# Performance work log

Measured on AMD Instinct MI355X. Metric: run time of the kernel, lower is better.

## Reference

```python
import jax, jax.numpy as jnp
import numpy as np

NUM_EXPERTS = 8

def setup_inputs() -> dict:
    key = jax.random.key(0)
    k1, k2, k3, k4, k5 = jax.random.split(key, 5)
    T, D, H, O, E, K = 4096, 1024, 2048, 1024, NUM_EXPERTS, 2
    hidden_states = jax.random.normal(k1, (T, D), dtype=jnp.float32)
    top_k_indices = jax.random.randint(k2, (T, K), 0, E, dtype=jnp.int64)
    top_k_weights = jax.random.uniform(k3, (T, K), dtype=jnp.float32)
    gate_up_proj = jax.random.normal(k4, (E, 2 * H, D), dtype=jnp.float32) * 0.02
    down_proj = jax.random.normal(k5, (E, O, H), dtype=jnp.float32) * 0.02
    return {
        "hidden_states": hidden_states,
        "top_k_indices": top_k_indices,
        "top_k_weights": top_k_weights,
        "gate_up_proj": gate_up_proj,
        "down_proj": down_proj,
    }


def _moe(hidden_states, top_k_weights, gate_up_proj, down_proj, top_k_indices):
    # Mathematically identical to the torch per-token-gather loop, expressed as
    # dense all-expert compute + sparse combine (non-selected experts get weight 0).
    T = hidden_states.shape[0]
    E = gate_up_proj.shape[0]
    # [T, E, 2H]
    gate_up = jnp.einsum('td,ehd->teh', hidden_states, gate_up_proj)
    gate, up = jnp.split(gate_up, 2, axis=-1)
    h = jax.nn.silu(gate) * up  # [T, E, H]
    expert_out = jnp.einsum('teh,eoh->teo', h, down_proj)  # [T, E, O]
    # combine weights: scatter top-k routing weights into [T, E]
    combine = jnp.zeros((T, E), dtype=hidden_states.dtype)
    rows = jnp.arange(T)[:, None]
    combine = combine.at[rows, top_k_indices].add(top_k_weights)
    return jnp.einsum('teo,te->to', expert_out, combine)


def reference(hidden_states, top_k_indices, top_k_weights, gate_up_proj, down_proj):
    return _moe(hidden_states, top_k_weights, gate_up_proj, down_proj, top_k_indices)
```

## Files before the change

### kernel.cpp

```cpp
#include <hip/hip_runtime.h>
#include <stdint.h>

#define TOKS 4096
#define DIM  1024
#define HID  2048
#define OUTD 1024
#define NE   8
#define MP   9216
#define NBR  72

typedef __bf16 bf16;
typedef bf16 bf16x8 __attribute__((ext_vector_type(8)));
typedef float f32x4 __attribute__((ext_vector_type(4)));
typedef __attribute__((address_space(1))) void gvoid;
typedef __attribute__((address_space(3))) void lvoid;

#define WGU_OFF  0ull
#define WD_OFF   (WGU_OFF + 67108864ull)
#define XG_OFF   (WD_OFF  + 33554432ull)
#define H_OFF    (XG_OFF  + 18874368ull)
#define TK_OFF   (H_OFF   + 37748736ull)
#define META_OFF (TK_OFF  + 36864ull)
#define T2S_OFF  (META_OFF + 1024ull)
#define O0_OFF   WGU_OFF
#define O1_OFF   (WGU_OFF + 18874368ull)

__device__ __forceinline__ unsigned short f2bf(float f) {
  union { float f; unsigned u; } v; v.f = f;
  unsigned r = (v.u + 0x7FFFu + ((v.u >> 16) & 1u)) >> 16;
  return (unsigned short)r;
}
__device__ __forceinline__ float bf2f(unsigned short h) {
  union { unsigned u; float f; } v; v.u = ((unsigned)h) << 16; return v.f;
}
__device__ __forceinline__ unsigned pack2(float a, float b) {
  return (unsigned)f2bf(a) | ((unsigned)f2bf(b) << 16);
}
__device__ __forceinline__ void cp16(const void* g, void* l) {
  __builtin_amdgcn_global_load_lds((gvoid*)(void*)g, (lvoid*)l, 16, 0, 0);
}

__global__ __launch_bounds__(1024) void route_kernel(const int* __restrict__ idx,
                                                     int* __restrict__ table,
                                                     int* __restrict__ slot_token,
                                                     int* __restrict__ tok2slot) {
  __shared__ int cnt[NE], offs[NE], cur[NE];
  const int tid = threadIdx.x, lane = tid & 63;
  for (int i = tid; i < MP; i += 1024) slot_token[i] = -1;
  if (tid < NE) cnt[tid] = 0;
  __syncthreads();
  int myE[8];
#pragma unroll
  for (int c = 0; c < 8; ++c) myE[c] = idx[c * 1024 + tid];
#pragma unroll
  for (int c = 0; c < 8; ++c) {
    int e = myE[c];
#pragma unroll
    for (int ex = 0; ex < NE; ++ex) {
      unsigned long long m = __ballot(e == ex);
      if (lane == 0 && m) atomicAdd(&cnt[ex], __popcll(m));
    }
  }
  __syncthreads();
  if (tid == 0) {
    int cum = 0;
    for (int e = 0; e < NE; ++e) {
      offs[e] = cum; cur[e] = 0;
      int nb = (cnt[e] + 127) >> 7;
      int bb = cum >> 7;
      for (int b = 0; b < nb; ++b) table[bb + b] = e;
      cum += nb << 7;
    }
    for (int b = cum >> 7; b < NBR; ++b) table[b] = -1;
  }
  __syncthreads();
#pragma unroll
  for (int c = 0; c < 8; ++c) {
    int e = myE[c];
    int pos = 0;
#pragma unroll
    for (int ex = 0; ex < NE; ++ex) {
      unsigned long long m = __ballot(e == ex);
      if (e == ex) {
        int rank = __popcll(m & ((1ull << lane) - 1ull));
        int leader = __ffsll(m) - 1;
        int base = 0;
        if (lane == leader) base = atomicAdd(&cur[ex], __popcll(m));
        base = __shfl(base, leader);
        pos = offs[ex] + base + rank;
      }
    }
    slot_token[pos] = (c * 1024 + tid) >> 1;
    tok2slot[c * 1024 + tid] = pos;
  }
}

#define GATHER_B 4608
__global__ void prep_kernel(const float* __restrict__ X, const int* __restrict__ slot_token,
                            uint4* __restrict__ Xg,
                            const float4* __restrict__ srcGu, uint2* __restrict__ dstGu,
                            const float4* __restrict__ srcD, uint2* __restrict__ dstD) {
  int bx = blockIdx.x;
  if (bx < GATHER_B) {
    int gid = bx * 256 + threadIdx.x;
    int row = gid >> 7, j = (gid & 127) << 3;
    int t = slot_token[row];
    uint4 o;
    if (t >= 0) {
      const float4* p = (const float4*)(X + (size_t)t * DIM + j);
      float4 a = p[0], b = p[1];
      o.x = pack2(a.x, a.y); o.y = pack2(a.z, a.w);
      o.z = pack2(b.x, b.y); o.w = pack2(b.z, b.w);
    } else {
      o = uint4{0u, 0u, 0u, 0u};
    }
    Xg[gid] = o;
  } else {
    const int n1 = NE * 2 * HID * DIM / 4;
    int i = (bx - GATHER_B) * 256 + threadIdx.x;
    float4 v; uint2* dp;
    if (i < n1) { v = srcGu[i]; dp = dstGu + i; }
    else        { v = srcD[i - n1]; dp = dstD + (i - n1); }
    uint2 o; o.x = pack2(v.x, v.y); o.y = pack2(v.z, v.w);
    *dp = o;
  }
}

__global__ void combine_kernel(const unsigned short* __restrict__ O0,
                               const unsigned short* __restrict__ O1,
                               const int* __restrict__ tok2slot,
                               const float* __restrict__ wts, float4* __restrict__ out) {
  int t = blockIdx.x, c = threadIdx.x;
  int s0 = tok2slot[2 * t], s1 = tok2slot[2 * t + 1];
  float w0 = wts[2 * t], w1 = wts[2 * t + 1];
  uint2 a0 = ((const uint2*)(O0 + (size_t)s0 * OUTD))[c];
  uint2 b0 = ((const uint2*)(O1 + (size_t)s0 * OUTD))[c];
  uint2 a1 = ((const uint2*)(O0 + (size_t)s1 * OUTD))[c];
  uint2 b1 = ((const uint2*)(O1 + (size_t)s1 * OUTD))[c];
  float4 o;
  o.x = w0 * (bf2f(a0.x & 0xFFFF) + bf2f(b0.x & 0xFFFF)) + w1 * (bf2f(a1.x & 0xFFFF) + bf2f(b1.x & 0xFFFF));
  o.y = w0 * (bf2f(a0.x >> 16)    + bf2f(b0.x >> 16))    + w1 * (bf2f(a1.x >> 16)    + bf2f(b1.x >> 16));
  o.z = w0 * (bf2f(a0.y & 0xFFFF) + bf2f(b0.y & 0xFFFF)) + w1 * (bf2f(a1.y & 0xFFFF) + bf2f(b1.y & 0xFFFF));
  o.w = w0 * (bf2f(a0.y >> 16)    + bf2f(b0.y >> 16))    + w1 * (bf2f(a1.y >> 16)    + bf2f(b1.y >> 16));
  out[(size_t)t * (OUTD / 4) + c] = o;
}

__global__ __launch_bounds__(256) void gemm1_kernel(
    const unsigned short* __restrict__ Xg,
    const unsigned short* __restrict__ Wgu,
    unsigned short* __restrict__ Hbuf,
    const int* __restrict__ table) {
  int e = table[blockIdx.y];
  if (e < 0) return;
  const int tid = threadIdx.x;
  const int lane = tid & 63, wave = tid >> 6;
  const int wm = wave >> 1, wn = wave & 1;
  const int lr = lane & 15, quad = lane >> 4;

  __shared__ bf16 As[128 * 64];
  __shared__ bf16 Bg[64 * 64];
  __shared__ bf16 Bu[64 * 64];

  const unsigned short* A_base  = Xg  + (size_t)blockIdx.y * 128 * DIM;
  const unsigned short* Wg_base = Wgu + (size_t)e * 2 * HID * DIM + (size_t)(blockIdx.x * 64) * DIM;
  const unsigned short* Wu_base = Wg_base + (size_t)HID * DIM;

  f32x4 accg[4][2] = {}; f32x4 accu[4][2] = {};

  for (int kt = 0; kt < DIM / 64; ++kt) {
    const int kb = kt * 64;
#pragma unroll
    for (int i = 0; i < 4; ++i) {
      int s = i * 256 + tid, row = s >> 3, pc = s & 7, gc = pc ^ (row & 7);
      cp16(A_base + (size_t)row * DIM + kb + gc * 8, (void*)(As + row * 64 + pc * 8));
    }
#pragma unroll
    for (int i = 0; i < 2; ++i) {
      int s = i * 256 + tid, row = s >> 3, pc = s & 7, gc = pc ^ (row & 7);
      cp16(Wg_base + (size_t)row * DIM + kb + gc * 8, (void*)(Bg + row * 64 + pc * 8));
      cp16(Wu_base + (size_t)row * DIM + kb + gc * 8, (void*)(Bu + row * 64 + pc * 8));
    }
    __syncthreads();
#pragma unroll
    for (int ks = 0; ks < 2; ++ks) {
      bf16x8 a[4], bg[2], bu[2];
#pragma unroll
      for (int i = 0; i < 4; ++i) {
        int row = wm * 64 + i * 16 + lr;
        int pc = (ks * 4 + quad) ^ (row & 7);
        a[i] = *(const bf16x8*)(As + row * 64 + pc * 8);
      }
#pragma unroll
      for (int j = 0; j < 2; ++j) {
        int row = wn * 32 + j * 16 + lr;
        int pc = (ks * 4 + quad) ^ (row & 7);
        bg[j] = *(const bf16x8*)(Bg + row * 64 + pc * 8);
        bu[j] = *(const bf16x8*)(Bu + row * 64 + pc * 8);
      }
#pragma unroll
      for (int i = 0; i < 4; ++i)
#pragma unroll
        for (int j = 0; j < 2; ++j) {
          accg[i][j] = __builtin_amdgcn_mfma_f32_16x16x32_bf16(a[i], bg[j], accg[i][j], 0, 0, 0);
          accu[i][j] = __builtin_amdgcn_mfma_f32_16x16x32_bf16(a[i], bu[j], accu[i][j], 0, 0, 0);
        }
    }
    __syncthreads();
  }

  const int rowBase = blockIdx.y * 128 + wm * 64;
  const int colBase = blockIdx.x * 64 + wn * 32;
#pragma unroll
  for (int i = 0; i < 4; ++i)
#pragma unroll
    for (int r = 0; r < 4; ++r) {
      int row = rowBase + i * 16 + quad * 4 + r;
#pragma unroll
      for (int j = 0; j < 2; ++j) {
        float g = accg[i][j][r], u = accu[i][j][r];
        float s = g / (1.0f + __expf(-g));
        Hbuf[(size_t)row * HID + colBase + j * 16 + lr] = f2bf(s * u);
      }
    }
}

__global__ __launch_bounds__(256) void gemm2_kernel(
    const unsigned short* __restrict__ Hbuf,
    const unsigned short* __restrict__ Wd,
    unsigned short* __restrict__ O0,
    unsigned short* __restrict__ O1,
    const int* __restrict__ table) {
  int e = table[blockIdx.y];
  if (e < 0) return;
  const int tid = threadIdx.x;
  const int lane = tid & 63, wave = tid >> 6;
  const int wm = wave >> 1, wn = wave & 1;
  const int lr = lane & 15, quad = lane >> 4;
  const int kslice = blockIdx.z;

  __shared__ bf16 As[128 * 64];
  __shared__ bf16 Bs[128 * 64];

  const unsigned short* A_base = Hbuf + (size_t)blockIdx.y * 128 * HID + kslice * (HID / 2);
  const unsigned short* B_base = Wd + (size_t)e * OUTD * HID + (size_t)(blockIdx.x * 128) * HID
                               + kslice * (HID / 2);

  f32x4 acc[4][4] = {};

  for (int kt = 0; kt < (HID / 2) / 64; ++kt) {
    const int kb = kt * 64;
#pragma unroll
    for (int i = 0; i < 4; ++i) {
      int s = i * 256 + tid, row = s >> 3, pc = s & 7, gc = pc ^ (row & 7);
      cp16(A_base + (size_t)row * HID + kb + gc * 8, (void*)(As + row * 64 + pc * 8));
      cp16(B_base + (size_t)row * HID + kb + gc * 8, (void*)(Bs + row * 64 + pc * 8));
    }
    __syncthreads();
#pragma unroll
    for (int ks = 0; ks < 2; ++ks) {
      bf16x8 a[4], b[4];
#pragma unroll
      for (int i = 0; i < 4; ++i) {
        int row = wm * 64 + i * 16 + lr;
        int pc = (ks * 4 + quad) ^ (row & 7);
        a[i] = *(const bf16x8*)(As + row * 64 + pc * 8);
      }
#pragma unroll
      for (int j = 0; j < 4; ++j) {
        int row = wn * 64 + j * 16 + lr;
        int pc = (ks * 4 + quad) ^ (row & 7);
        b[j] = *(const bf16x8*)(Bs + row * 64 + pc * 8);
      }
#pragma unroll
      for (int i = 0; i < 4; ++i)
#pragma unroll
        for (int j = 0; j < 4; ++j)
          acc[i][j] = __builtin_amdgcn_mfma_f32_16x16x32_bf16(a[i], b[j], acc[i][j], 0, 0, 0);
    }
    __syncthreads();
  }

  unsigned short* O = kslice ? O1 : O0;
  const int rowBase = blockIdx.y * 128 + wm * 64;
  const int colBase = blockIdx.x * 128 + wn * 64;
#pragma unroll
  for (int i = 0; i < 4; ++i)
#pragma unroll
    for (int r = 0; r < 4; ++r) {
      int row = rowBase + i * 16 + quad * 4 + r;
      unsigned short* Orow = O + (size_t)row * OUTD + colBase;
#pragma unroll
      for (int j = 0; j < 4; ++j)
        Orow[j * 16 + lr] = f2bf(acc[i][j][r]);
    }
}

extern "C" void kernel_launch(void* const* d_in, const int* in_sizes, int n_in,
                              void* d_out, int out_size, void* d_ws, size_t ws_size,
                              hipStream_t stream) {
  const float* X     = (const float*)d_in[0];
  const int*   idx   = (const int*)d_in[1];
  const float* wts   = (const float*)d_in[2];
  const float* WguF  = (const float*)d_in[3];
  const float* WdF   = (const float*)d_in[4];
  float* out = (float*)d_out;

  char* base = (char*)d_ws;
  unsigned short* Wgu = (unsigned short*)(base + WGU_OFF);
  unsigned short* Wd  = (unsigned short*)(base + WD_OFF);
  unsigned short* Xg  = (unsigned short*)(base + XG_OFF);
  unsigned short* Hb  = (unsigned short*)(base + H_OFF);
  unsigned short* O0  = (unsigned short*)(base + O0_OFF);
  unsigned short* O1  = (unsigned short*)(base + O1_OFF);
  int* slot_token = (int*)(base + TK_OFF);
  int* table      = (int*)(base + META_OFF);
  int* tok2slot   = (int*)(base + T2S_OFF);

  route_kernel<<<1, 1024, 0, stream>>>(idx, table, slot_token, tok2slot);
  {
    const int convB = (NE * 2 * HID * DIM + NE * OUTD * HID) / 4 / 256;
    prep_kernel<<<GATHER_B + convB, 256, 0, stream>>>(X, slot_token, (uint4*)Xg,
        (const float4*)WguF, (uint2*)Wgu, (const float4*)WdF, (uint2*)Wd);
  }
  gemm1_kernel<<<dim3(HID / 64, NBR), 256, 0, stream>>>(Xg, Wgu, Hb, table);
  gemm2_kernel<<<dim3(OUTD / 128, NBR, 2), 256, 0, stream>>>(Hb, Wd, O0, O1, table);
  combine_kernel<<<TOKS, 256, 0, stream>>>(O0, O1, tok2slot, wts, (float4*)out);
}
```

Baseline: 434.4 us.

## Double-buffer LDS in expert GEMMs and merge weight conversion into routing launch

Both grouped GEMMs now use two LDS buffers so the global-to-LDS copies for the next K tile are issued before computing the current one, aiming to hide load latency. The fp32-to-bf16 weight conversion is moved into the routing launch so it runs alongside the single-block routing work, and the token gather becomes a separate kernel. Doubled LDS usage may lower occupancy per CU.

Result: slower. 452.2 us (+4.1%).

```diff
diff --git a/kernel.cpp b/kernel.cpp
--- a/kernel.cpp
+++ b/kernel.cpp
@@ -40,10 +40,22 @@
   __builtin_amdgcn_global_load_lds((gvoid*)(void*)g, (lvoid*)l, 16, 0, 0);
 }
 
-__global__ __launch_bounds__(1024) void route_kernel(const int* __restrict__ idx,
-                                                     int* __restrict__ table,
-                                                     int* __restrict__ slot_token,
-                                                     int* __restrict__ tok2slot) {
+#define CONVB ((NE * 2 * HID * DIM + NE * OUTD * HID) / 4 / 1024)
+__global__ __launch_bounds__(1024) void route_conv_kernel(
+    const int* __restrict__ idx, int* __restrict__ table,
+    int* __restrict__ slot_token, int* __restrict__ tok2slot,
+    const float4* __restrict__ srcGu, uint2* __restrict__ dstGu,
+    const float4* __restrict__ srcD, uint2* __restrict__ dstD) {
+  if (blockIdx.x != 0) {
+    const int n1 = NE * 2 * HID * DIM / 4;
+    int i = (int)(blockIdx.x - 1) * 1024 + threadIdx.x;
+    float4 v; uint2* dp;
+    if (i < n1) { v = srcGu[i]; dp = dstGu + i; }
+    else        { v = srcD[i - n1]; dp = dstD + (i - n1); }
+    uint2 o; o.x = pack2(v.x, v.y); o.y = pack2(v.z, v.w);
+    *dp = o;
+    return;
+  }
   __shared__ int cnt[NE], offs[NE], cur[NE];
   const int tid = threadIdx.x, lane = tid & 63;
   for (int i = tid; i < MP; i += 1024) slot_token[i] = -1;
@@ -96,34 +108,22 @@
 }
 
 #define GATHER_B 4608
-__global__ void prep_kernel(const float* __restrict__ X, const int* __restrict__ slot_token,
-                            uint4* __restrict__ Xg,
-                            const float4* __restrict__ srcGu, uint2* __restrict__ dstGu,
-                            const float4* __restrict__ srcD, uint2* __restrict__ dstD) {
-  int bx = blockIdx.x;
-  if (bx < GATHER_B) {
-    int gid = bx * 256 + threadIdx.x;
-    int row = gid >> 7, j = (gid & 127) << 3;
-    int t = slot_token[row];
-    uint4 o;
-    if (t >= 0) {
-      const float4* p = (const float4*)(X + (size_t)t * DIM + j);
-      float4 a = p[0], b = p[1];
-      o.x = pack2(a.x, a.y); o.y = pack2(a.z, a.w);
-      o.z = pack2(b.x, b.y); o.w = pack2(b.z, b.w);
-    } else {
-      o = uint4{0u, 0u, 0u, 0u};
-    }
-    Xg[gid] = o;
+__global__ void gather_kernel(const float* __restrict__ X,
+                              const int* __restrict__ slot_token,
+                              uint4* __restrict__ Xg) {
+  int gid = blockIdx.x * 256 + threadIdx.x;
+  int row = gid >> 7, j = (gid & 127) << 3;
+  int t = slot_token[row];
+  uint4 o;
+  if (t >= 0) {
+    const float4* p = (const float4*)(X + (size_t)t * DIM + j);
+    float4 a = p[0], b = p[1];
+    o.x = pack2(a.x, a.y); o.y = pack2(a.z, a.w);
+    o.z = pack2(b.x, b.y); o.w = pack2(b.z, b.w);
   } else {
-    const int n1 = NE * 2 * HID * DIM / 4;
-    int i = (bx - GATHER_B) * 256 + threadIdx.x;
-    float4 v; uint2* dp;
-    if (i < n1) { v = srcGu[i]; dp = dstGu + i; }
-    else        { v = srcD[i - n1]; dp = dstD + (i - n1); }
-    uint2 o; o.x = pack2(v.x, v.y); o.y = pack2(v.z, v.w);
-    *dp = o;
-  }
+    o = uint4{0u, 0u, 0u, 0u};
+  }
+  Xg[gid] = o;
 }
 
 __global__ void combine_kernel(const unsigned short* __restrict__ O0,
@@ -157,9 +157,9 @@
   const int wm = wave >> 1, wn = wave & 1;
   const int lr = lane & 15, quad = lane >> 4;
 
-  __shared__ bf16 As[128 * 64];
-  __shared__ bf16 Bg[64 * 64];
-  __shared__ bf16 Bu[64 * 64];
+  __shared__ bf16 As[2][128 * 64];
+  __shared__ bf16 Bg[2][64 * 64];
+  __shared__ bf16 Bu[2][64 * 64];
 
   const unsigned short* A_base  = Xg  + (size_t)blockIdx.y * 128 * DIM;
   const unsigned short* Wg_base = Wgu + (size_t)e * 2 * HID * DIM + (size_t)(blockIdx.x * 64) * DIM;
@@ -167,20 +167,22 @@
 
   f32x4 accg[4][2] = {}; f32x4 accu[4][2] = {};
 
-  for (int kt = 0; kt < DIM / 64; ++kt) {
+  auto stage = [&](int buf, int kt) {
     const int kb = kt * 64;
 #pragma unroll
     for (int i = 0; i < 4; ++i) {
       int s = i * 256 + tid, row = s >> 3, pc = s & 7, gc = pc ^ (row & 7);
-      cp16(A_base + (size_t)row * DIM + kb + gc * 8, (void*)(As + row * 64 + pc * 8));
+      cp16(A_base + (size_t)row * DIM + kb + gc * 8, (void*)(&As[buf][row * 64 + pc * 8]));
     }
 #pragma unroll
     for (int i = 0; i < 2; ++i) {
       int s = i * 256 + tid, row = s >> 3, pc = s & 7, gc = pc ^ (row & 7);
-      cp16(Wg_base + (size_t)row * DIM + kb + gc * 8, (void*)(Bg + row * 64 + pc * 8));
-      cp16(Wu_base + (size_t)row * DIM + kb + gc * 8, (void*)(Bu + row * 64 + pc * 8));
-    }
-    __syncthreads();
+      cp16(Wg_base + (size_t)row * DIM + kb + gc * 8, (void*)(&Bg[buf][row * 64 + pc * 8]));
+      cp16(Wu_base + (size_t)row * DIM + kb + gc * 8, (void*)(&Bu[buf][row * 64 + pc * 8]));
+    }
+  };
+
+  auto compute = [&](int buf) {
 #pragma unroll
     for (int ks = 0; ks < 2; ++ks) {
       bf16x8 a[4], bg[2], bu[2];
@@ -188,14 +190,14 @@
       for (int i = 0; i < 4; ++i) {
         int row = wm * 64 + i * 16 + lr;
         int pc = (ks * 4 + quad) ^ (row & 7);
-        a[i] = *(const bf16x8*)(As + row * 64 + pc * 8);
+        a[i] = *(const bf16x8*)(&As[buf][row * 64 + pc * 8]);
       }
 #pragma unroll
       for (int j = 0; j < 2; ++j) {
         int row = wn * 32 + j * 16 + lr;
         int pc = (ks * 4 + quad) ^ (row & 7);
-        bg[j] = *(const bf16x8*)(Bg + row * 64 + pc * 8);
-        bu[j] = *(const bf16x8*)(Bu + row * 64 + pc * 8);
+        bg[j] = *(const bf16x8*)(&Bg[buf][row * 64 + pc * 8]);
+        bu[j] = *(const bf16x8*)(&Bu[buf][row * 64 + pc * 8]);
       }
 #pragma unroll
       for (int i = 0; i < 4; ++i)
@@ -205,6 +207,17 @@
           accu[i][j] = __builtin_amdgcn_mfma_f32_16x16x32_bf16(a[i], bu[j], accu[i][j], 0, 0, 0);
         }
     }
+  };
+
+  stage(0, 0);
+  __syncthreads();
+#pragma unroll 1
+  for (int kt = 0; kt < DIM / 64; kt += 2) {
+    stage(1, kt + 1);
+    compute(0);
+    __syncthreads();
+    if (kt + 2 < DIM / 64) stage(0, kt + 2);
+    compute(1);
     __syncthreads();
   }
 
@@ -238,8 +251,8 @@
   const int lr = lane & 15, quad = lane >> 4;
   const int kslice = blockIdx.z;
 
-  __shared__ bf16 As[128 * 64];
-  __shared__ bf16 Bs[128 * 64];
+  __shared__ bf16 As[2][128 * 64];
+  __shared__ bf16 Bs[2][128 * 64];
 
   const unsigned short* A_base = Hbuf + (size_t)blockIdx.y * 128 * HID + kslice * (HID / 2);
   const unsigned short* B_base = Wd + (size_t)e * OUTD * HID + (size_t)(blockIdx.x * 128) * HID
@@ -247,15 +260,17 @@
 
   f32x4 acc[4][4] = {};
 
-  for (int kt = 0; kt < (HID / 2) / 64; ++kt) {
+  auto stage = [&](int buf, int kt) {
     const int kb = kt * 64;
 #pragma unroll
     for (int i = 0; i < 4; ++i) {
       int s = i * 256 + tid, row = s >> 3, pc = s & 7, gc = pc ^ (row & 7);
-      cp16(A_base + (size_t)row * HID + kb + gc * 8, (void*)(As + row * 64 + pc * 8));
-      cp16(B_base + (size_t)row * HID + kb + gc * 8, (void*)(Bs + row * 64 + pc * 8));
-    }
-    __syncthreads();
+      cp16(A_base + (size_t)row * HID + kb + gc * 8, (void*)(&As[buf][row * 64 + pc * 8]));
+      cp16(B_base + (size_t)row * HID + kb + gc * 8, (void*)(&Bs[buf][row * 64 + pc * 8]));
+    }
+  };
+
+  auto compute = [&](int buf) {
 #pragma unroll
     for (int ks = 0; ks < 2; ++ks) {
       bf16x8 a[4], b[4];
@@ -263,13 +278,13 @@
       for (int i = 0; i < 4; ++i) {
         int row = wm * 64 + i * 16 + lr;
         int pc = (ks * 4 + quad) ^ (row & 7);
-        a[i] = *(const bf16x8*)(As + row * 64 + pc * 8);
+        a[i] = *(const bf16x8*)(&As[buf][row * 64 + pc * 8]);
       }
 #pragma unroll
       for (int j = 0; j < 4; ++j) {
         int row = wn * 64 + j * 16 + lr;
         int pc = (ks * 4 + quad) ^ (row & 7);
-        b[j] = *(const bf16x8*)(Bs + row * 64 + pc * 8);
+        b[j] = *(const bf16x8*)(&Bs[buf][row * 64 + pc * 8]);
       }
 #pragma unroll
       for (int i = 0; i < 4; ++i)
@@ -277,6 +292,17 @@
         for (int j = 0; j < 4; ++j)
           acc[i][j] = __builtin_amdgcn_mfma_f32_16x16x32_bf16(a[i], b[j], acc[i][j], 0, 0, 0);
     }
+  };
+
+  stage(0, 0);
+  __syncthreads();
+#pragma unroll 1
+  for (int kt = 0; kt < (HID / 2) / 64; kt += 2) {
+    stage(1, kt + 1);
+    compute(0);
+    __syncthreads();
+    if (kt + 2 < (HID / 2) / 64) stage(0, kt + 2);
+    compute(1);
     __syncthreads();
   }
 
@@ -316,12 +342,9 @@
   int* table      = (int*)(base + META_OFF);
   int* tok2slot   = (int*)(base + T2S_OFF);
 
-  route_kernel<<<1, 1024, 0, stream>>>(idx, table, slot_token, tok2slot);
-  {
-    const int convB = (NE * 2 * HID * DIM + NE * OUTD * HID) / 4 / 256;
-    prep_kernel<<<GATHER_B + convB, 256, 0, stream>>>(X, slot_token, (uint4*)Xg,
-        (const float4*)WguF, (uint2*)Wgu, (const float4*)WdF, (uint2*)Wd);
-  }
+  route_conv_kernel<<<1 + CONVB, 1024, 0, stream>>>(idx, table, slot_token, tok2slot,
+      (const float4*)WguF, (uint2*)Wgu, (const float4*)WdF, (uint2*)Wd);
+  gather_kernel<<<GATHER_B, 256, 0, stream>>>(X, slot_token, (uint4*)Xg);
   gemm1_kernel<<<dim3(HID / 64, NBR), 256, 0, stream>>>(Xg, Wgu, Hb, table);
   gemm2_kernel<<<dim3(OUTD / 128, NBR, 2), 256, 0, stream>>>(Hb, Wd, O0, O1, table);
   combine_kernel<<<TOKS, 256, 0, stream>>>(O0, O1, tok2slot, wts, (float4*)out);
```
